# Optimization experiments

Hardware: AMD Instinct MI355X
Metric: run time of the kernel (lower is better)

## Reference

```python
import jax, jax.numpy as jnp
import numpy as np

K = 3
STRIDE = 1
PAD = 1
DIL = 1
EPS = 1e-5


def setup_inputs() -> dict:
    key = jax.random.key(0)
    k1, k2, k3 = jax.random.split(key, 3)
    B, Cin, H, W = 8, 128, 64, 64
    Cout = 256
    x = jax.random.normal(k1, (B, Cin, H, W), dtype=jnp.float32)
    # Offset conv is zero-initialized in the original; use small random weights
    # so the deformable sampling path is actually exercised (offsets ~ +-1 px).
    offset_w = jax.random.normal(k2, (2 * K * K, Cin, K, K), dtype=jnp.float32) * 0.01
    offset_b = jnp.zeros((2 * K * K,), dtype=jnp.float32)
    dconv_w = jax.random.normal(k3, (Cout, Cin, K, K), dtype=jnp.float32) * 0.05
    dconv_b = jnp.zeros((Cout,), dtype=jnp.float32)
    bn_gamma = jnp.ones((Cout,), dtype=jnp.float32)
    bn_beta = jnp.zeros((Cout,), dtype=jnp.float32)
    return {"x": x, "offset_w": offset_w, "offset_b": offset_b,
            "dconv_w": dconv_w, "dconv_b": dconv_b,
            "bn_gamma": bn_gamma, "bn_beta": bn_beta}


def _conv2d(x, w, b):
    y = jax.lax.conv_general_dilated(
        x, w, window_strides=(STRIDE, STRIDE),
        padding=[(PAD, PAD), (PAD, PAD)], rhs_dilation=(DIL, DIL),
        dimension_numbers=("NCHW", "OIHW", "NCHW"))
    return y + b[None, :, None, None]


def _bilinear_gather(x, sy, sx):
    # x: [B,C,H,W]; sy,sx: [B,KK,Ho,Wo] float sample coords (zero-pad outside).
    B, C, H, W = x.shape
    xf = x.reshape(B, C, H * W)

    def corner(yi, xi, w):
        valid = (yi >= 0) & (yi < H) & (xi >= 0) & (xi < W)
        idx = (jnp.clip(yi, 0, H - 1) * W + jnp.clip(xi, 0, W - 1)).reshape(B, -1)
        v = jnp.take_along_axis(xf, idx[:, None, :], axis=2)  # [B,C,KK*Ho*Wo]
        return v * (w * valid).reshape(B, 1, -1)

    y0 = jnp.floor(sy).astype(jnp.int32)
    x0 = jnp.floor(sx).astype(jnp.int32)
    wy = sy - y0
    wx = sx - x0
    val = (corner(y0, x0, (1 - wy) * (1 - wx))
           + corner(y0, x0 + 1, (1 - wy) * wx)
           + corner(y0 + 1, x0, wy * (1 - wx))
           + corner(y0 + 1, x0 + 1, wy * wx))
    return val.reshape((B, C) + sy.shape[1:])  # [B,C,KK,Ho,Wo]


def reference(x, offset_w, offset_b, dconv_w, dconv_b, bn_gamma, bn_beta):
    # 1) offset conv
    offset = _conv2d(x, offset_w, offset_b)           # [B, 2*K*K, Ho, Wo]
    B, _, Ho, Wo = offset.shape
    off = offset.reshape(B, K * K, 2, Ho, Wo)         # (dy, dx) per kernel tap

    # 2) deformable sampling positions
    kidx = jnp.arange(K * K)
    ky = (kidx // K) * DIL
    kx = (kidx % K) * DIL
    base_y = (jnp.arange(Ho) * STRIDE - PAD)[None, :, None] + ky[:, None, None]  # [KK,Ho,1]
    base_x = (jnp.arange(Wo) * STRIDE - PAD)[None, None, :] + kx[:, None, None]  # [KK,1,Wo]
    sy = base_y[None] + off[:, :, 0]                  # [B,KK,Ho,Wo]
    sx = base_x[None] + off[:, :, 1]

    patches = _bilinear_gather(x, sy, sx)             # [B,Cin,KK,Ho,Wo]

    # 3) deformable conv = contraction of patches with weight
    Cout = dconv_w.shape[0]
    wflat = dconv_w.reshape(Cout, dconv_w.shape[1], K * K)
    y = jnp.einsum("bckhw,ock->bohw", patches, wflat) + dconv_b[None, :, None, None]

    # 4) BatchNorm (training-mode batch stats, biased variance) + SiLU
    mean = jnp.mean(y, axis=(0, 2, 3), keepdims=True)
    var = jnp.var(y, axis=(0, 2, 3), keepdims=True)
    y = (y - mean) * jax.lax.rsqrt(var + EPS)
    y = y * bn_gamma[None, :, None, None] + bn_beta[None, :, None, None]
    return jax.nn.silu(y)
```

## Files before the change

### kernel.cpp

```cpp
#include <hip/hip_runtime.h>
#include <hip/hip_bf16.h>
#include <math.h>

#define B_    8
#define CIN   128
#define Hx    64
#define Wx    64
#define COUT  256
#define HW    4096
#define KTOT  1152
#define NOFF  18
#define M_    32768
#define OFFSEG (B_ * NOFF * HW)
#define NCH   36

typedef short bf16x8 __attribute__((ext_vector_type(8)));
typedef float f32x4  __attribute__((ext_vector_type(4)));
typedef unsigned short us8 __attribute__((ext_vector_type(8)));

typedef __attribute__((address_space(1))) const unsigned int gu32;
typedef __attribute__((address_space(3))) unsigned int lu32;
static __device__ __forceinline__ void async_cp16(const short* g, short* l) {
  __builtin_amdgcn_global_load_lds((gu32*)g, (lu32*)l, 16, 0, 0);
}

static __device__ __forceinline__ short f2bf(float f) {
  __hip_bfloat16 h = __float2bfloat16(f);
  return *reinterpret_cast<short*>(&h);
}

static __device__ __forceinline__ float b2f(unsigned short u) {
  unsigned int v = ((unsigned int)u) << 16;
  return __uint_as_float(v);
}

__global__ __launch_bounds__(256, 4) void pre_kernel(
    const float* __restrict__ x, const float* __restrict__ ow,
    const float* __restrict__ ob, float* __restrict__ offp,
    const float* __restrict__ dw, short* __restrict__ Wb) {
  __shared__ __align__(16) float lds_w[16 * 9 * 12];
  int blk = blockIdx.x;
  int tid = threadIdx.x;
  if (blk >= 1024) {
    int t = (blk - 1024) * 256 + tid;
    int ki = t & 31;
    int cout = (t >> 5) & 255;
    int kc = t >> 13;
    int k = kc * 32 + ki;
    int kk = k >> 7, cin = k & 127;
    Wb[t] = f2bf(dw[(cout * CIN + cin) * 9 + kk]);
    return;
  }
  int r = blk & 63, seg = (blk >> 6) & 7, chalf = blk >> 9;
  for (int i = tid; i < 16 * 9 * 12; i += 256) {
    int t = i % 12;
    int rem = i / 12;
    int ch = rem % 9, ci = rem / 9;
    lds_w[i] = (t < 9) ? ow[(chalf * 9 + ch) * KTOT + (seg * 16 + ci) * 9 + t] : 0.f;
  }
  __syncthreads();

  int v = r * 256 + tid;
  int wp = v & 31, ho = (v >> 5) & 63, b = v >> 11;
  int wo0 = wp * 2;
  float acc0[9], acc1[9];
#pragma unroll
  for (int c = 0; c < 9; ++c) { acc0[c] = 0.f; acc1[c] = 0.f; }
  const float* xb = x + (b * CIN + seg * 16) * HW;
  for (int ci = 0; ci < 16; ++ci) {
    const float* xp = xb + ci * HW;
    float win[3][4];
#pragma unroll
    for (int ky = 0; ky < 3; ++ky) {
      int iy = ho - 1 + ky;
      bool rok = (iy >= 0) & (iy < Hx);
      const float* rowp = xp + iy * Wx;
#pragma unroll
      for (int c = 0; c < 4; ++c) {
        int ix = wo0 - 1 + c;
        win[ky][c] = (rok & (ix >= 0) & (ix < Wx)) ? rowp[ix] : 0.f;
      }
    }
    const float4* wq = (const float4*)&lds_w[ci * 108];
#pragma unroll
    for (int ch = 0; ch < 9; ++ch) {
      float4 w0 = wq[ch * 3 + 0];
      float4 w1 = wq[ch * 3 + 1];
      float4 w2 = wq[ch * 3 + 2];
      float a0 = acc0[ch], a1 = acc1[ch];
      a0 = fmaf(win[0][0], w0.x, a0); a1 = fmaf(win[0][1], w0.x, a1);
      a0 = fmaf(win[0][1], w0.y, a0); a1 = fmaf(win[0][2], w0.y, a1);
      a0 = fmaf(win[0][2], w0.z, a0); a1 = fmaf(win[0][3], w0.z, a1);
      a0 = fmaf(win[1][0], w0.w, a0); a1 = fmaf(win[1][1], w0.w, a1);
      a0 = fmaf(win[1][1], w1.x, a0); a1 = fmaf(win[1][2], w1.x, a1);
      a0 = fmaf(win[1][2], w1.y, a0); a1 = fmaf(win[1][3], w1.y, a1);
      a0 = fmaf(win[2][0], w1.z, a0); a1 = fmaf(win[2][1], w1.z, a1);
      a0 = fmaf(win[2][1], w1.w, a0); a1 = fmaf(win[2][2], w1.w, a1);
      a0 = fmaf(win[2][2], w2.x, a0); a1 = fmaf(win[2][3], w2.x, a1);
      acc0[ch] = a0; acc1[ch] = a1;
    }
  }
  float* op = offp + seg * OFFSEG + (b * NOFF + chalf * 9) * HW + ho * 64 + wo0;
#pragma unroll
  for (int c = 0; c < 9; ++c) {
    float bias = (seg == 0) ? ob[chalf * 9 + c] : 0.f;
    op[c * HW]     = acc0[c] + bias;
    op[c * HW + 1] = acc1[c] + bias;
  }
}

__global__ __launch_bounds__(256) void coeff_kernel(
    const float* __restrict__ offp, short4* __restrict__ cidx, float4* __restrict__ cwt) {
  int t = blockIdx.x * 256 + threadIdx.x;
  int m = t & (M_ - 1);
  int kk = t >> 15;
  int b = m >> 12, ho = (m >> 6) & 63, wo = m & 63;
  int base = (b * NOFF + 2 * kk) * HW + (m & 4095);
  int base2 = base + HW;
  float dy = 0.f, dx = 0.f;
#pragma unroll
  for (int s = 0; s < 8; ++s) {
    dy += offp[base + s * OFFSEG];
    dx += offp[base2 + s * OFFSEG];
  }
  float sy = (float)(ho - 1 + kk / 3) + dy;
  float sx = (float)(wo - 1 + kk % 3) + dx;
  float fy = floorf(sy), fx = floorf(sx);
  int y0 = (int)fy, x0 = (int)fx;
  float wy = sy - fy, wx = sx - fx;
  int y1 = y0 + 1, x1 = x0 + 1;
  int cy0 = min(max(y0, 0), Hx - 1), cy1 = min(max(y1, 0), Hx - 1);
  int cx0 = min(max(x0, 0), Wx - 1), cx1 = min(max(x1, 0), Wx - 1);
  bool vy0 = (y0 >= 0) & (y0 < Hx), vy1 = (y1 >= 0) & (y1 < Hx);
  bool vx0 = (x0 >= 0) & (x0 < Wx), vx1 = (x1 >= 0) & (x1 < Wx);
  short4 id;
  id.x = (short)(cy0 * Wx + cx0); id.y = (short)(cy0 * Wx + cx1);
  id.z = (short)(cy1 * Wx + cx0); id.w = (short)(cy1 * Wx + cx1);
  float4 wv;
  wv.x = (vy0 && vx0) ? (1.f - wy) * (1.f - wx) : 0.f;
  wv.y = (vy0 && vx1) ? (1.f - wy) * wx : 0.f;
  wv.z = (vy1 && vx0) ? wy * (1.f - wx) : 0.f;
  wv.w = (vy1 && vx1) ? wy * wx : 0.f;
  cidx[t] = id;
  cwt[t] = wv;
}

__global__ __launch_bounds__(256) void sampler_kernel(
    const float* __restrict__ x, const short4* __restrict__ cidx,
    const float4* __restrict__ cwt, short* __restrict__ Pb) {
  __shared__ __align__(16) us8 ldsp[HW];
  int blk = blockIdx.x;
  int b = blk & 7;
  int g8 = (blk >> 3) & 15;
  int posq = blk >> 7;
  int cinq = g8 >> 2;
  int e8 = g8 & 3;
  int tid = threadIdx.x;

  const float* p0 = x + (b * CIN + g8 * 8) * HW;
#pragma unroll
  for (int it = 0; it < 16; ++it) {
    int p = it * 256 + tid;
    us8 pk;
#pragma unroll
    for (int c = 0; c < 8; ++c)
      pk[c] = (unsigned short)f2bf(p0[c * HW + p]);
    ldsp[p] = pk;
  }
  __syncthreads();

  const int pbase = b * HW + posq * 1024 + tid;
  for (int kk = 0; kk < 9; ++kk) {
    int kcg = kk * 4 + cinq;
    const short4* cp = cidx + kk * M_ + pbase;
    const float4* wp = cwt + kk * M_ + pbase;
    short* pb = Pb + (kcg * M_ + pbase) * 32 + e8 * 8;
#pragma unroll
    for (int it = 0; it < 4; ++it) {
      short4 id = cp[it * 256];
      float4 wv = wp[it * 256];
      us8 A  = ldsp[(int)id.x];
      us8 Bv = ldsp[(int)id.y];
      us8 C  = ldsp[(int)id.z];
      us8 D  = ldsp[(int)id.w];
      union { short s[8]; int4 v; } bu;
#pragma unroll
      for (int c = 0; c < 8; ++c) {
        float s = wv.x * b2f(A[c]) + wv.y * b2f(Bv[c])
                + wv.z * b2f(C[c]) + wv.w * b2f(D[c]);
        bu.s[c] = f2bf(s);
      }
      *(int4*)&pb[it * 256 * 32] = bu.v;
    }
  }
}

__global__ __launch_bounds__(256, 2) void gemm_kernel(
    const short* __restrict__ Wb, const short* __restrict__ Pb,
    float* __restrict__ y, float* __restrict__ psum, float* __restrict__ psq) {
  __shared__ __align__(16) short lds[2][8192];

  int tid = threadIdx.x;
  int mt = blockIdx.x & 255;
  int ct = blockIdx.x >> 8;
  int cout0 = ct * 128;
  int m0 = mt * 128;

  int lane = tid & 63, wave = tid >> 6;
  int quad = lane >> 4, l16 = lane & 15;
  int wm = (wave & 1) << 6;
  int wnm = (wave >> 1) << 6;

  int isB = wave >> 1;
  int sub = wave & 1;
  const short* srcbase = isB ? (Pb + m0 * 32) : (Wb + cout0 * 32);
  const int sstride = isB ? (M_ * 32) : (256 * 32);
  const int soff = sub * 2048 + lane * 8;
  const int doff = isB * 4096 + sub * 2048 + lane * 8;

  f32x4 zero = {0.f, 0.f, 0.f, 0.f};
  f32x4 acc[4][4];
#pragma unroll
  for (int i = 0; i < 4; ++i)
#pragma unroll
    for (int j = 0; j < 4; ++j) acc[i][j] = zero;

  {
    const short* s = srcbase + soff;
    short* d = &lds[0][doff];
#pragma unroll
    for (int j = 0; j < 4; ++j)
      async_cp16(s + j * 512, d + j * 512);
  }

  for (int ch = 0; ch < NCH; ++ch) {
    int p = ch & 1;
    __syncthreads();
    if (ch < NCH - 1) {
      const short* s = srcbase + (ch + 1) * sstride + soff;
      short* d = &lds[p ^ 1][doff];
#pragma unroll
      for (int j = 0; j < 4; ++j)
        async_cp16(s + j * 512, d + j * 512);
    }
    const short* sa = &lds[p][0];
    const short* sb = &lds[p][4096];
    bf16x8 af[4], bfr[4];
#pragma unroll
    for (int i = 0; i < 4; ++i)
      af[i] = *(const bf16x8*)&sa[(wm + i * 16 + l16) * 32 + quad * 8];
#pragma unroll
    for (int j = 0; j < 4; ++j)
      bfr[j] = *(const bf16x8*)&sb[(wnm + j * 16 + l16) * 32 + quad * 8];
#pragma unroll
    for (int i = 0; i < 4; ++i)
#pragma unroll
      for (int j = 0; j < 4; ++j)
        acc[i][j] = __builtin_amdgcn_mfma_f32_16x16x32_bf16(af[i], bfr[j], acc[i][j], 0, 0, 0);
  }

#pragma unroll
  for (int i = 0; i < 4; ++i) {
    int crow = cout0 + wm + i * 16 + quad * 4;
#pragma unroll
    for (int j = 0; j < 4; ++j) {
      int m = m0 + wnm + j * 16 + l16;
      int b = m >> 12;
      float* yp = y + (b * COUT + crow) * HW + (m & 4095);
#pragma unroll
      for (int r2 = 0; r2 < 4; ++r2)
        yp[r2 * HW] = acc[i][j][r2];
    }
  }

  __syncthreads();
  float* redsum = (float*)&lds[0][0];
  float* redsq  = redsum + 256;
#pragma unroll
  for (int i = 0; i < 4; ++i) {
#pragma unroll
    for (int r2 = 0; r2 < 4; ++r2) {
      float s = 0.f, q = 0.f;
#pragma unroll
      for (int j = 0; j < 4; ++j) {
        float v = acc[i][j][r2];
        s += v;
        q = fmaf(v, v, q);
      }
#pragma unroll
      for (int o = 8; o > 0; o >>= 1) {
        s += __shfl_down(s, o);
        q += __shfl_down(q, o);
      }
      if (l16 == 0) {
        int cl = wm + i * 16 + quad * 4 + r2;
        int half = wave >> 1;
        redsum[half * 128 + cl] = s;
        redsq [half * 128 + cl] = q;
      }
    }
  }
  __syncthreads();
  if (tid < 128) {
    float s = redsum[tid] + redsum[128 + tid];
    float q = redsq [tid] + redsq [128 + tid];
    psum[(cout0 + tid) * 256 + mt] = s;
    psq [(cout0 + tid) * 256 + mt] = q;
  }
}

__global__ __launch_bounds__(256) void bn_finalize_kernel(
    const float* __restrict__ psum, const float* __restrict__ psq,
    float* __restrict__ mean, float* __restrict__ invstd) {
  int c = blockIdx.x;
  int tid = threadIdx.x;
  float s = psum[c * 256 + tid];
  float q = psq[c * 256 + tid];
#pragma unroll
  for (int o = 32; o > 0; o >>= 1) {
    s += __shfl_down(s, o);
    q += __shfl_down(q, o);
  }
  __shared__ float rs[4], rq[4];
  int wid = tid >> 6, ln = tid & 63;
  if (ln == 0) { rs[wid] = s; rq[wid] = q; }
  __syncthreads();
  if (tid == 0) {
    float S = rs[0] + rs[1] + rs[2] + rs[3];
    float Q = rq[0] + rq[1] + rq[2] + rq[3];
    float m = S / 32768.f;
    mean[c] = m;
    invstd[c] = rsqrtf(Q / 32768.f - m * m + 1e-5f);
  }
}

__global__ __launch_bounds__(256) void bn_silu_kernel(
    float* __restrict__ y, const float* __restrict__ mean,
    const float* __restrict__ invstd, const float* __restrict__ gamma,
    const float* __restrict__ beta) {
  int i4 = blockIdx.x * 256 + threadIdx.x;
  int c = (i4 >> 10) & 255;
  float4 v = ((const float4*)y)[i4];
  float m = mean[c], sc = invstd[c] * gamma[c], bt = beta[c];
  float t0 = (v.x - m) * sc + bt;
  float t1 = (v.y - m) * sc + bt;
  float t2 = (v.z - m) * sc + bt;
  float t3 = (v.w - m) * sc + bt;
  float4 o;
  o.x = t0 / (1.f + expf(-t0));
  o.y = t1 / (1.f + expf(-t1));
  o.z = t2 / (1.f + expf(-t2));
  o.w = t3 / (1.f + expf(-t3));
  ((float4*)y)[i4] = o;
}

extern "C" void kernel_launch(void* const* d_in, const int* in_sizes, int n_in,
                              void* d_out, int out_size, void* d_ws, size_t ws_size,
                              hipStream_t stream) {
  const float* x     = (const float*)d_in[0];
  const float* ow    = (const float*)d_in[1];
  const float* ob    = (const float*)d_in[2];
  const float* dw    = (const float*)d_in[3];
  const float* gamma = (const float*)d_in[5];
  const float* beta  = (const float*)d_in[6];
  float* y = (float*)d_out;

  float*  ws   = (float*)d_ws;
  short*  Pb   = (short*)ws;
  float*  offp = ws + 18874368;
  short4* cidx = (short4*)(ws + 23592960);
  float4* cwt  = (float4*)(ws + 24182784);
  short*  Wb   = (short*)(ws + 25362432);
  float*  mean   = ws + 25509888;
  float*  invstd = ws + 25510144;
  float*  psum   = ws + 25510400;
  float*  psq    = ws + 25575936;

  pre_kernel<<<2176, 256, 0, stream>>>(x, ow, ob, offp, dw, Wb);
  coeff_kernel<<<1152, 256, 0, stream>>>(offp, cidx, cwt);
  sampler_kernel<<<512, 256, 0, stream>>>(x, cidx, cwt, Pb);
  gemm_kernel<<<512, 256, 0, stream>>>(Wb, Pb, y, psum, psq);
  bn_finalize_kernel<<<256, 256, 0, stream>>>(psum, psq, mean, invstd);
  bn_silu_kernel<<<8192, 256, 0, stream>>>(y, mean, invstd, gamma, beta);
}
```

Baseline: 182.6 us.

## Fuse GEMM, BN statistics finalize and BN+SiLU via cooperative grid sync

Merges the GEMM, BN finalize and BN+SiLU kernels into one cooperative kernel. Accumulators stay in registers across two grid-wide syncs, so normalization and SiLU are applied before a single write of y. This removes the fp32 y round trip through global memory (one write plus one read and write) and two kernel launches. It requires all 512 blocks to be co-resident at two blocks per CU and adds the cost of the grid barriers.

```diff
diff --git a/kernel.cpp b/kernel.cpp
--- a/kernel.cpp
+++ b/kernel.cpp
@@ -1,6 +1,9 @@
 #include <hip/hip_runtime.h>
 #include <hip/hip_bf16.h>
+#include <hip/hip_cooperative_groups.h>
 #include <math.h>
+
+namespace cg = cooperative_groups;
 
 #define B_    8
 #define CIN   128
@@ -195,9 +198,11 @@
   }
 }
 
-__global__ __launch_bounds__(256, 2) void gemm_kernel(
+__global__ __launch_bounds__(256, 2) void gemm_bn_kernel(
     const short* __restrict__ Wb, const short* __restrict__ Pb,
-    float* __restrict__ y, float* __restrict__ psum, float* __restrict__ psq) {
+    float* __restrict__ y, float* __restrict__ psum, float* __restrict__ psq,
+    const float* __restrict__ gamma, const float* __restrict__ beta,
+    float* __restrict__ mean, float* __restrict__ invstd) {
   __shared__ __align__(16) short lds[2][8192];
 
   int tid = threadIdx.x;
@@ -259,20 +264,6 @@
         acc[i][j] = __builtin_amdgcn_mfma_f32_16x16x32_bf16(af[i], bfr[j], acc[i][j], 0, 0, 0);
   }
 
-#pragma unroll
-  for (int i = 0; i < 4; ++i) {
-    int crow = cout0 + wm + i * 16 + quad * 4;
-#pragma unroll
-    for (int j = 0; j < 4; ++j) {
-      int m = m0 + wnm + j * 16 + l16;
-      int b = m >> 12;
-      float* yp = y + (b * COUT + crow) * HW + (m & 4095);
-#pragma unroll
-      for (int r2 = 0; r2 < 4; ++r2)
-        yp[r2 * HW] = acc[i][j][r2];
-    }
-  }
-
   __syncthreads();
   float* redsum = (float*)&lds[0][0];
   float* redsq  = redsum + 256;
@@ -307,51 +298,63 @@
     psum[(cout0 + tid) * 256 + mt] = s;
     psq [(cout0 + tid) * 256 + mt] = q;
   }
-}
-
-__global__ __launch_bounds__(256) void bn_finalize_kernel(
-    const float* __restrict__ psum, const float* __restrict__ psq,
-    float* __restrict__ mean, float* __restrict__ invstd) {
-  int c = blockIdx.x;
-  int tid = threadIdx.x;
-  float s = psum[c * 256 + tid];
-  float q = psq[c * 256 + tid];
-#pragma unroll
-  for (int o = 32; o > 0; o >>= 1) {
-    s += __shfl_down(s, o);
-    q += __shfl_down(q, o);
-  }
-  __shared__ float rs[4], rq[4];
-  int wid = tid >> 6, ln = tid & 63;
-  if (ln == 0) { rs[wid] = s; rq[wid] = q; }
-  __syncthreads();
-  if (tid == 0) {
-    float S = rs[0] + rs[1] + rs[2] + rs[3];
-    float Q = rq[0] + rq[1] + rq[2] + rq[3];
-    float m = S / 32768.f;
-    mean[c] = m;
-    invstd[c] = rsqrtf(Q / 32768.f - m * m + 1e-5f);
-  }
-}
-
-__global__ __launch_bounds__(256) void bn_silu_kernel(
-    float* __restrict__ y, const float* __restrict__ mean,
-    const float* __restrict__ invstd, const float* __restrict__ gamma,
-    const float* __restrict__ beta) {
-  int i4 = blockIdx.x * 256 + threadIdx.x;
-  int c = (i4 >> 10) & 255;
-  float4 v = ((const float4*)y)[i4];
-  float m = mean[c], sc = invstd[c] * gamma[c], bt = beta[c];
-  float t0 = (v.x - m) * sc + bt;
-  float t1 = (v.y - m) * sc + bt;
-  float t2 = (v.z - m) * sc + bt;
-  float t3 = (v.w - m) * sc + bt;
-  float4 o;
-  o.x = t0 / (1.f + expf(-t0));
-  o.y = t1 / (1.f + expf(-t1));
-  o.z = t2 / (1.f + expf(-t2));
-  o.w = t3 / (1.f + expf(-t3));
-  ((float4*)y)[i4] = o;
+
+  cg::grid_group grid = cg::this_grid();
+  __threadfence();
+  grid.sync();
+
+  if (blockIdx.x < 256) {
+    int c = blockIdx.x;
+    float s = psum[c * 256 + tid];
+    float q = psq [c * 256 + tid];
+#pragma unroll
+    for (int o = 32; o > 0; o >>= 1) {
+      s += __shfl_down(s, o);
+      q += __shfl_down(q, o);
+    }
+    float* rs = (float*)&lds[0][0];
+    float* rq = rs + 4;
+    int wid = tid >> 6, ln = tid & 63;
+    if (ln == 0) { rs[wid] = s; rq[wid] = q; }
+    __syncthreads();
+    if (tid == 0) {
+      float S = rs[0] + rs[1] + rs[2] + rs[3];
+      float Q = rq[0] + rq[1] + rq[2] + rq[3];
+      float m = S / 32768.f;
+      mean[c] = m;
+      invstd[c] = rsqrtf(Q / 32768.f - m * m + 1e-5f);
+    }
+  }
+  __threadfence();
+  grid.sync();
+
+  float* scb = (float*)&lds[0][0];
+  float* btb = scb + 128;
+  __syncthreads();
+  if (tid < 128) {
+    int c = cout0 + tid;
+    float m = mean[c];
+    float sc = invstd[c] * gamma[c];
+    scb[tid] = sc;
+    btb[tid] = fmaf(-m, sc, beta[c]);
+  }
+  __syncthreads();
+#pragma unroll
+  for (int i = 0; i < 4; ++i) {
+    int crow = cout0 + wm + i * 16 + quad * 4;
+#pragma unroll
+    for (int j = 0; j < 4; ++j) {
+      int m = m0 + wnm + j * 16 + l16;
+      int b = m >> 12;
+      float* yp = y + (b * COUT + crow) * HW + (m & 4095);
+#pragma unroll
+      for (int r2 = 0; r2 < 4; ++r2) {
+        int cl = wm + i * 16 + quad * 4 + r2;
+        float t = fmaf(acc[i][j][r2], scb[cl], btb[cl]);
+        yp[r2 * HW] = t / (1.f + expf(-t));
+      }
+    }
+  }
 }
 
 extern "C" void kernel_launch(void* const* d_in, const int* in_sizes, int n_in,
@@ -379,7 +382,9 @@
   pre_kernel<<<2176, 256, 0, stream>>>(x, ow, ob, offp, dw, Wb);
   coeff_kernel<<<1152, 256, 0, stream>>>(offp, cidx, cwt);
   sampler_kernel<<<512, 256, 0, stream>>>(x, cidx, cwt, Pb);
-  gemm_kernel<<<512, 256, 0, stream>>>(Wb, Pb, y, psum, psq);
-  bn_finalize_kernel<<<256, 256, 0, stream>>>(psum, psq, mean, invstd);
-  bn_silu_kernel<<<8192, 256, 0, stream>>>(y, mean, invstd, gamma, beta);
-}
+
+  void* kargs[] = {(void*)&Wb, (void*)&Pb, (void*)&y, (void*)&psum, (void*)&psq,
+                   (void*)&gamma, (void*)&beta, (void*)&mean, (void*)&invstd};
+  hipLaunchCooperativeKernel((const void*)gemm_bn_kernel, dim3(512), dim3(256),
+                             kargs, 0, stream);
+}
```

Result: slower. 398.2 us (+118.1%).
